# Optimization experiments

Measured on AMD Instinct MI355X. Metric: run time of the kernel, lower is better.

The kernel has to match this reference:

```python
import jax, jax.numpy as jnp
import numpy as np

EPS = 1e-12  # torch F.normalize clamp_min eps

def _l2_normalize(x):
    n = jnp.linalg.norm(x, axis=-1, keepdims=True)
    return x / jnp.maximum(n, EPS)

def setup_inputs() -> dict:
    key = jax.random.key(0)
    k1, k2 = jax.random.split(key)
    z_e = jax.random.normal(k1, (32, 256, 32, 32), dtype=jnp.float32)
    weight = jax.random.normal(k2, (1024, 256), dtype=jnp.float32)
    return {"z_e": z_e, "weight": weight}

def reference(z_e, weight):
    B, C, H, W = z_e.shape  # C == embedding_dim
    z = jnp.transpose(z_e, (0, 2, 3, 1))            # [B,H,W,C]
    flat = _l2_normalize(z.reshape(-1, C))          # [N,C]
    w_n = _l2_normalize(weight)                     # [K,C]
    # distances = 2 - 2 * <flat, w_n>; computed without grad in original
    dist = 2.0 - 2.0 * jnp.matmul(flat, w_n.T)      # [N,K]
    idx = jnp.argmin(dist, axis=1)                  # [N]
    z_q = w_n[idx].reshape(B, H, W, C)              # gather codebook rows
    z_q = jnp.transpose(z_q, (0, 3, 1, 2))          # [B,C,H,W]
    indices = idx.reshape(B, H, W)
    return z_q, indices
```

## Files before the change

### kernel.cpp

```cpp
#include <hip/hip_runtime.h>


typedef _Float16 half8 __attribute__((ext_vector_type(8)));
typedef _Float16 half4 __attribute__((ext_vector_type(4)));
typedef float    floatx4 __attribute__((ext_vector_type(4)));

#define C_DIM 256
#define K_CODES 1024
#define HW 1024
#define NPIX 32768
#define NTILES 8
#define USTR 520

#define GLOAD_LDS16(g, l) __builtin_amdgcn_global_load_lds(                    \
    (const __attribute__((address_space(1))) unsigned int*)(g),                \
    (__attribute__((address_space(3))) unsigned int*)(l), 16, 0, 0)

__global__ __launch_bounds__(256) void vq_norm_w(const float* __restrict__ w,
                                                 float* __restrict__ w_n,
                                                 _Float16* __restrict__ wh,
                                                 _Float16* __restrict__ wl) {
    const int row = blockIdx.x;
    const int t   = threadIdx.x;
    float x = w[row * C_DIM + t];
    float s = x * x;
    #pragma unroll
    for (int off = 32; off > 0; off >>= 1) s += __shfl_down(s, off, 64);
    __shared__ float wsum[4];
    if ((t & 63) == 0) wsum[t >> 6] = s;
    __syncthreads();
    float tot = wsum[0] + wsum[1] + wsum[2] + wsum[3];
    float inv = 1.0f / fmaxf(sqrtf(tot), 1e-12f);
    float y = x * inv;
    w_n[row * C_DIM + t] = y;
    float ys = 16.0f * y;
    _Float16 hi = (_Float16)ys;
    wh[row * C_DIM + t] = hi;
    wl[row * C_DIM + t] = (_Float16)(ys - (float)hi);
}

__global__ __launch_bounds__(256, 4) void vq_gemm(
        const float* __restrict__ z,
        const _Float16* __restrict__ wh, const _Float16* __restrict__ wl,
        float* __restrict__ cand_val, int* __restrict__ cand_idx) {
    __shared__ _Float16 Ah[8 * USTR], Al[8 * USTR];
    __shared__ _Float16 Bh[8 * USTR], Bl[8 * USTR];
    __shared__ float red_v[128][2];
    __shared__ int   red_i[128][2];

    const int tid  = threadIdx.x;
    const int lane = tid & 63, wave = tid >> 6;
    const int wm = wave >> 1, wn = wave & 1;
    const int quad = lane >> 4, l15 = lane & 15;
    const int m0 = blockIdx.x * 128, n0 = blockIdx.y * 128;
    const int b  = m0 >> 10, p0 = m0 & 1023;

    const _Float16* bsrc = (wave < 2) ? wh : wl;
    _Float16*       bdst = (wave < 2) ? Bh : Bl;
    const int ub = (wave & 1) * 4;
    const _Float16* gB[4];
    _Float16*       lB[4];
    #pragma unroll
    for (int i = 0; i < 4; i++) {
        gB[i] = bsrc + (size_t)(n0 + (ub + i) * 16 + l15) * C_DIM + quad * 8;
        lB[i] = bdst + (ub + i) * USTR;
    }

    const int ap = (lane & 31) * 4;
    const int as = lane >> 5;
    const int ak = wave * 8 + as * 4;
    const float* zA = z + ((size_t)b * C_DIM + ak) * HW + p0 + ap;

    floatx4 acc[4][4];
    #pragma unroll
    for (int i = 0; i < 4; i++)
        #pragma unroll
        for (int j = 0; j < 4; j++) acc[i][j] = (floatx4){0.f, 0.f, 0.f, 0.f};

    const int afrag = wm * 4, bfrag = wn * 4;

    for (int kt = 0; kt < 8; kt++) {
        __syncthreads();
        #pragma unroll
        for (int i = 0; i < 4; i++)
            GLOAD_LDS16(gB[i] + kt * 32, lB[i]);
        floatx4 za[4];
        #pragma unroll
        for (int r = 0; r < 4; r++)
            za[r] = *(const floatx4*)(zA + (size_t)(kt * 32 + r) * HW);
        #pragma unroll
        for (int i = 0; i < 4; i++) {
            half4 hv, lv;
            #pragma unroll
            for (int r = 0; r < 4; r++) {
                float xv = 4.0f * za[r][i];
                _Float16 h = (_Float16)xv;
                hv[r] = h;
                lv[r] = (_Float16)(xv - (float)h);
            }
            const int p = ap + i;
            const int aidx = (p >> 4) * USTR + wave * 128 + (p & 15) * 8 + as * 4;
            *(half4*)&Ah[aidx] = hv;
            *(half4*)&Al[aidx] = lv;
        }
        __syncthreads();

        half8 ah[4], al[4], bh[4], bl[4];
        #pragma unroll
        for (int i = 0; i < 4; i++) {
            ah[i] = *(const half8*)&Ah[(afrag + i) * USTR + lane * 8];
            al[i] = *(const half8*)&Al[(afrag + i) * USTR + lane * 8];
            bh[i] = *(const half8*)&Bh[(bfrag + i) * USTR + lane * 8];
            bl[i] = *(const half8*)&Bl[(bfrag + i) * USTR + lane * 8];
        }
        #pragma unroll
        for (int mi = 0; mi < 4; mi++)
            #pragma unroll
            for (int ni = 0; ni < 4; ni++) {
                acc[mi][ni] = __builtin_amdgcn_mfma_f32_16x16x32_f16(ah[mi], bh[ni], acc[mi][ni], 0, 0, 0);
                acc[mi][ni] = __builtin_amdgcn_mfma_f32_16x16x32_f16(ah[mi], bl[ni], acc[mi][ni], 0, 0, 0);
                acc[mi][ni] = __builtin_amdgcn_mfma_f32_16x16x32_f16(al[mi], bh[ni], acc[mi][ni], 0, 0, 0);
            }
    }

    #pragma unroll
    for (int mi = 0; mi < 4; mi++) {
        #pragma unroll
        for (int r = 0; r < 4; r++) {
            float bv = -__builtin_inff();
            int   bi = 0x7fffffff;
            #pragma unroll
            for (int ni = 0; ni < 4; ni++) {
                float v = acc[mi][ni][r];
                int  ci = n0 + wn * 64 + ni * 16 + l15;
                if (v > bv || (v == bv && ci < bi)) { bv = v; bi = ci; }
            }
            #pragma unroll
            for (int mk = 8; mk; mk >>= 1) {
                float ov = __shfl_xor(bv, mk, 16);
                int   oi = __shfl_xor(bi, mk, 16);
                if (ov > bv || (ov == bv && oi < bi)) { bv = ov; bi = oi; }
            }
            if (l15 == 0) {
                int row = wm * 64 + mi * 16 + quad * 4 + r;
                red_v[row][wn] = bv;
                red_i[row][wn] = bi;
            }
        }
    }
    __syncthreads();
    if (tid < 128) {
        float bv = red_v[tid][0]; int bi = red_i[tid][0];
        float v2 = red_v[tid][1]; int i2 = red_i[tid][1];
        if (v2 > bv || (v2 == bv && i2 < bi)) { bv = v2; bi = i2; }
        const int pix = m0 + tid;
        cand_val[(size_t)pix * NTILES + blockIdx.y] = bv;
        cand_idx[(size_t)pix * NTILES + blockIdx.y] = bi;
    }
}

__global__ __launch_bounds__(256) void vq_finalize(
        const float* __restrict__ cand_val,
        const int*   __restrict__ cand_idx,
        const float* __restrict__ w_n,
        float* __restrict__ zq,
        float* __restrict__ idx_out) {
    __shared__ float tile[64][257];
    __shared__ int   idx_s[64];
    const int t    = threadIdx.x;
    const int lane = t & 63, wave = t >> 6;
    const int n0   = blockIdx.x * 64;
    const int b    = n0 >> 10, p0 = n0 & 1023;

    if (t < 64) {
        const int n = n0 + t;
        const size_t base = (size_t)n * NTILES;
        float bv = cand_val[base]; int bi = cand_idx[base];
        #pragma unroll
        for (int j = 1; j < NTILES; j++) {
            float v = cand_val[base + j];
            int   c = cand_idx[base + j];
            if (v > bv || (v == bv && c < bi)) { bv = v; bi = c; }
        }
        idx_s[t] = bi;
        idx_out[n] = (float)bi;
    }
    __syncthreads();
    #pragma unroll
    for (int i = 0; i < 16; i++) {
        const int p = wave * 16 + i;
        const int row = idx_s[p];
        floatx4 v = *(const floatx4*)(w_n + (size_t)row * C_DIM + lane * 4);
        *(floatx4*)&tile[p][lane * 4] = v;
    }
    __syncthreads();
    float* zqb = zq + (size_t)b * (C_DIM * HW) + p0;
    #pragma unroll
    for (int it = 0; it < 16; it++) {
        const int c = it * 16 + wave * 4 + (lane >> 4);
        const int p = (lane & 15) * 4;
        floatx4 v = { tile[p][c], tile[p + 1][c], tile[p + 2][c], tile[p + 3][c] };
        *(floatx4*)(zqb + (size_t)c * HW + p) = v;
    }
}

extern "C" void kernel_launch(void* const* d_in, const int* in_sizes, int n_in,
                              void* d_out, int out_size, void* d_ws, size_t ws_size,
                              hipStream_t stream) {
    const float* z = (const float*)d_in[0];
    const float* w = (const float*)d_in[1];
    float* out     = (float*)d_out;

    char* ws = (char*)d_ws;
    float*    w_n  = (float*)(ws);
    _Float16* wh   = (_Float16*)(ws + (1u << 20));
    _Float16* wl   = (_Float16*)(ws + (3u << 19));
    float*    cval = (float*)(ws + (2u << 20));
    int*      cidx = (int*)(ws + (3u << 20));

    vq_norm_w<<<K_CODES, 256, 0, stream>>>(w, w_n, wh, wl);
    vq_gemm<<<dim3(NPIX / 128, NTILES), 256, 0, stream>>>(z, wh, wl, cval, cidx);
    vq_finalize<<<NPIX / 64, 256, 0, stream>>>(cval, cidx, w_n, out, out + 8388608);
}
```

Baseline: 157.4 us.

## Pre-split z into fp16 hi/lo in prep kernel and double-buffer GEMM LDS

New measurement: 194.1 us. 23.3% more time.

```diff
diff --git a/kernel.cpp b/kernel.cpp
--- a/kernel.cpp
+++ b/kernel.cpp
@@ -2,7 +2,6 @@
 
 
 typedef _Float16 half8 __attribute__((ext_vector_type(8)));
-typedef _Float16 half4 __attribute__((ext_vector_type(4)));
 typedef float    floatx4 __attribute__((ext_vector_type(4)));
 
 #define C_DIM 256
@@ -10,41 +9,87 @@
 #define HW 1024
 #define NPIX 32768
 #define NTILES 8
-#define USTR 520
+#define USTR 512
 
 #define GLOAD_LDS16(g, l) __builtin_amdgcn_global_load_lds(                    \
     (const __attribute__((address_space(1))) unsigned int*)(g),                \
     (__attribute__((address_space(3))) unsigned int*)(l), 16, 0, 0)
 
-__global__ __launch_bounds__(256) void vq_norm_w(const float* __restrict__ w,
-                                                 float* __restrict__ w_n,
-                                                 _Float16* __restrict__ wh,
-                                                 _Float16* __restrict__ wl) {
-    const int row = blockIdx.x;
-    const int t   = threadIdx.x;
-    float x = w[row * C_DIM + t];
-    float s = x * x;
-    #pragma unroll
-    for (int off = 32; off > 0; off >>= 1) s += __shfl_down(s, off, 64);
+__global__ __launch_bounds__(256) void vq_prep(
+        const float* __restrict__ z, const float* __restrict__ w,
+        float* __restrict__ w_n, _Float16* __restrict__ wh, _Float16* __restrict__ wl,
+        _Float16* __restrict__ zh, _Float16* __restrict__ zl) {
     __shared__ float wsum[4];
-    if ((t & 63) == 0) wsum[t >> 6] = s;
-    __syncthreads();
-    float tot = wsum[0] + wsum[1] + wsum[2] + wsum[3];
-    float inv = 1.0f / fmaxf(sqrtf(tot), 1e-12f);
-    float y = x * inv;
-    w_n[row * C_DIM + t] = y;
-    float ys = 16.0f * y;
-    _Float16 hi = (_Float16)ys;
-    wh[row * C_DIM + t] = hi;
-    wl[row * C_DIM + t] = (_Float16)(ys - (float)hi);
-}
-
-__global__ __launch_bounds__(256, 4) void vq_gemm(
-        const float* __restrict__ z,
+    __shared__ unsigned pk[64][257];
+    const int t = threadIdx.x;
+
+    if (blockIdx.x < K_CODES) {
+        const int row = blockIdx.x;
+        float x = w[row * C_DIM + t];
+        float s = x * x;
+        #pragma unroll
+        for (int off = 32; off > 0; off >>= 1) s += __shfl_down(s, off, 64);
+        if ((t & 63) == 0) wsum[t >> 6] = s;
+        __syncthreads();
+        float tot = wsum[0] + wsum[1] + wsum[2] + wsum[3];
+        float inv = 1.0f / fmaxf(sqrtf(tot), 1e-12f);
+        float y = x * inv;
+        w_n[row * C_DIM + t] = y;
+        float ys = 16.0f * y;
+        _Float16 hi = (_Float16)ys;
+        wh[row * C_DIM + t] = hi;
+        wl[row * C_DIM + t] = (_Float16)(ys - (float)hi);
+        return;
+    }
+
+    const int zb = blockIdx.x - K_CODES;
+    const int pg = zb * 64;
+    const int b  = pg >> 10, p0 = pg & 1023;
+    const float* zp = z + (size_t)b * C_DIM * HW + p0;
+
+    const int cc = t >> 4, pp = (t & 15) * 4;
+    #pragma unroll
+    for (int it = 0; it < 16; it++) {
+        const int c = it * 16 + cc;
+        floatx4 v = *(const floatx4*)(zp + (size_t)c * HW + pp);
+        #pragma unroll
+        for (int j = 0; j < 4; j++) {
+            float xs = 4.0f * v[j];
+            _Float16 h = (_Float16)xs;
+            _Float16 l = (_Float16)(xs - (float)h);
+            pk[pp + j][c] = (unsigned)__builtin_bit_cast(unsigned short, h)
+                          | ((unsigned)__builtin_bit_cast(unsigned short, l) << 16);
+        }
+    }
+    __syncthreads();
+
+    const int pl = t >> 4, c0 = (t & 15) * 16;
+    #pragma unroll
+    for (int it = 0; it < 4; it++) {
+        const int p = it * 16 + pl;
+        half8 hv0, hv1, lv0, lv1;
+        #pragma unroll
+        for (int s = 0; s < 8; s++) {
+            unsigned u0 = pk[p][c0 + s];
+            unsigned u1 = pk[p][c0 + 8 + s];
+            hv0[s] = __builtin_bit_cast(_Float16, (unsigned short)(u0 & 0xffffu));
+            lv0[s] = __builtin_bit_cast(_Float16, (unsigned short)(u0 >> 16));
+            hv1[s] = __builtin_bit_cast(_Float16, (unsigned short)(u1 & 0xffffu));
+            lv1[s] = __builtin_bit_cast(_Float16, (unsigned short)(u1 >> 16));
+        }
+        const size_t base = (size_t)(pg + p) * C_DIM + c0;
+        *(half8*)(zh + base)     = hv0;
+        *(half8*)(zh + base + 8) = hv1;
+        *(half8*)(zl + base)     = lv0;
+        *(half8*)(zl + base + 8) = lv1;
+    }
+}
+
+__global__ __launch_bounds__(256, 2) void vq_gemm(
+        const _Float16* __restrict__ zh, const _Float16* __restrict__ zl,
         const _Float16* __restrict__ wh, const _Float16* __restrict__ wl,
         float* __restrict__ cand_val, int* __restrict__ cand_idx) {
-    __shared__ _Float16 Ah[8 * USTR], Al[8 * USTR];
-    __shared__ _Float16 Bh[8 * USTR], Bl[8 * USTR];
+    __shared__ _Float16 S[2][4][8 * USTR];
     __shared__ float red_v[128][2];
     __shared__ int   red_i[128][2];
 
@@ -53,23 +98,12 @@
     const int wm = wave >> 1, wn = wave & 1;
     const int quad = lane >> 4, l15 = lane & 15;
     const int m0 = blockIdx.x * 128, n0 = blockIdx.y * 128;
-    const int b  = m0 >> 10, p0 = m0 & 1023;
-
-    const _Float16* bsrc = (wave < 2) ? wh : wl;
-    _Float16*       bdst = (wave < 2) ? Bh : Bl;
-    const int ub = (wave & 1) * 4;
-    const _Float16* gB[4];
-    _Float16*       lB[4];
-    #pragma unroll
-    for (int i = 0; i < 4; i++) {
-        gB[i] = bsrc + (size_t)(n0 + (ub + i) * 16 + l15) * C_DIM + quad * 8;
-        lB[i] = bdst + (ub + i) * USTR;
-    }
-
-    const int ap = (lane & 31) * 4;
-    const int as = lane >> 5;
-    const int ak = wave * 8 + as * 4;
-    const float* zA = z + ((size_t)b * C_DIM + ak) * HW + p0 + ap;
+
+    const _Float16* ph = (wave & 2) ? wh : zh;
+    const _Float16* pl_ = (wave & 2) ? wl : zl;
+    const _Float16* pbase = (wave & 1) ? pl_ : ph;
+    const int rbase = (wave & 2) ? n0 : m0;
+    const _Float16* gsrc = pbase + (size_t)(rbase + l15) * C_DIM + quad * 8;
 
     floatx4 acc[4][4];
     #pragma unroll
@@ -79,40 +113,30 @@
 
     const int afrag = wm * 4, bfrag = wn * 4;
 
+    #define STAGE(kt, nb)                                                      \
+        {   const _Float16* g_ = gsrc + (kt) * 32;                             \
+            _Float16* l_ = &S[(nb)][wave][0];                                  \
+            _Pragma("unroll")                                                  \
+            for (int u = 0; u < 8; u++)                                        \
+                GLOAD_LDS16(g_ + (size_t)u * (16 * C_DIM), l_ + u * USTR);     \
+        }
+
+    STAGE(0, 0);
+    int cur = 0;
+    #pragma unroll
     for (int kt = 0; kt < 8; kt++) {
         __syncthreads();
-        #pragma unroll
-        for (int i = 0; i < 4; i++)
-            GLOAD_LDS16(gB[i] + kt * 32, lB[i]);
-        floatx4 za[4];
-        #pragma unroll
-        for (int r = 0; r < 4; r++)
-            za[r] = *(const floatx4*)(zA + (size_t)(kt * 32 + r) * HW);
+        if (kt < 7) STAGE(kt + 1, cur ^ 1);
+
+        half8 ah[4], al[4], bh[4], bl[4];
         #pragma unroll
         for (int i = 0; i < 4; i++) {
-            half4 hv, lv;
-            #pragma unroll
-            for (int r = 0; r < 4; r++) {
-                float xv = 4.0f * za[r][i];
-                _Float16 h = (_Float16)xv;
-                hv[r] = h;
-                lv[r] = (_Float16)(xv - (float)h);
-            }
-            const int p = ap + i;
-            const int aidx = (p >> 4) * USTR + wave * 128 + (p & 15) * 8 + as * 4;
-            *(half4*)&Ah[aidx] = hv;
-            *(half4*)&Al[aidx] = lv;
-        }
-        __syncthreads();
-
-        half8 ah[4], al[4], bh[4], bl[4];
-        #pragma unroll
-        for (int i = 0; i < 4; i++) {
-            ah[i] = *(const half8*)&Ah[(afrag + i) * USTR + lane * 8];
-            al[i] = *(const half8*)&Al[(afrag + i) * USTR + lane * 8];
-            bh[i] = *(const half8*)&Bh[(bfrag + i) * USTR + lane * 8];
-            bl[i] = *(const half8*)&Bl[(bfrag + i) * USTR + lane * 8];
-        }
+            ah[i] = *(const half8*)&S[cur][0][(afrag + i) * USTR + lane * 8];
+            al[i] = *(const half8*)&S[cur][1][(afrag + i) * USTR + lane * 8];
+            bh[i] = *(const half8*)&S[cur][2][(bfrag + i) * USTR + lane * 8];
+            bl[i] = *(const half8*)&S[cur][3][(bfrag + i) * USTR + lane * 8];
+        }
+        __builtin_amdgcn_s_setprio(1);
         #pragma unroll
         for (int mi = 0; mi < 4; mi++)
             #pragma unroll
@@ -121,7 +145,10 @@
                 acc[mi][ni] = __builtin_amdgcn_mfma_f32_16x16x32_f16(ah[mi], bl[ni], acc[mi][ni], 0, 0, 0);
                 acc[mi][ni] = __builtin_amdgcn_mfma_f32_16x16x32_f16(al[mi], bh[ni], acc[mi][ni], 0, 0, 0);
             }
-    }
+        __builtin_amdgcn_s_setprio(0);
+        cur ^= 1;
+    }
+    #undef STAGE
 
     #pragma unroll
     for (int mi = 0; mi < 4; mi++) {
@@ -212,13 +239,15 @@
     float* out     = (float*)d_out;
 
     char* ws = (char*)d_ws;
-    float*    w_n  = (float*)(ws);
-    _Float16* wh   = (_Float16*)(ws + (1u << 20));
-    _Float16* wl   = (_Float16*)(ws + (3u << 19));
-    float*    cval = (float*)(ws + (2u << 20));
-    int*      cidx = (int*)(ws + (3u << 20));
-
-    vq_norm_w<<<K_CODES, 256, 0, stream>>>(w, w_n, wh, wl);
-    vq_gemm<<<dim3(NPIX / 128, NTILES), 256, 0, stream>>>(z, wh, wl, cval, cidx);
+    _Float16* zh   = (_Float16*)(ws);
+    _Float16* zl   = (_Float16*)(ws + (16u << 20));
+    float*    w_n  = (float*)(ws + (32u << 20));
+    _Float16* wh   = (_Float16*)(ws + (33u << 20));
+    _Float16* wl   = (_Float16*)(ws + (33u << 20) + (1u << 19));
+    float*    cval = (float*)(ws + (34u << 20));
+    int*      cidx = (int*)(ws + (35u << 20));
+
+    vq_prep<<<K_CODES + NPIX / 64, 256, 0, stream>>>(z, w, w_n, wh, wl, zh, zl);
+    vq_gemm<<<dim3(NPIX / 128, NTILES), 256, 0, stream>>>(zh, zl, wh, wl, cval, cidx);
     vq_finalize<<<NPIX / 64, 256, 0, stream>>>(cval, cidx, w_n, out, out + 8388608);
 }
```
